# Kernel optimization log

Measured on AMD Instinct MI355X. Metric: run time of the kernel, lower is better.

Reference implementation:

```python
import jax, jax.numpy as jnp
import numpy as np

E = 1_000_000      # number of edges
N_NODE = 200_000   # nodes in this layer's frontier
IN_DIM = 64
ATTN_DIM = 64
OUT_DIM = 64
N_REL = 200
N_ENT = 50_000
B = 8              # batchsize


def setup_inputs() -> dict:
    key = jax.random.key(0)
    ks = jax.random.split(key, 16)
    # edges columns: [r_idx, _, rel, _, sub, obj]
    r_idx = jax.random.randint(ks[0], (E,), 0, B)
    rel = jax.random.randint(ks[1], (E,), 0, 2 * N_REL + 1)
    sub = jax.random.randint(ks[2], (E,), 0, N_NODE)
    obj = jax.random.randint(ks[3], (E,), 0, N_NODE)
    zeros = jnp.zeros((E,), dtype=jnp.int64 if jax.config.jax_enable_x64 else jnp.int32)
    edges = jnp.stack([r_idx, zeros, rel, zeros, sub, obj], axis=1)

    q_sub = jax.random.randint(ks[4], (B,), 0, N_ENT)
    q_rel = jax.random.randint(ks[5], (B,), 0, 2 * N_REL + 1)
    hidden = jax.random.normal(ks[6], (N_NODE, IN_DIM), dtype=jnp.float32)
    nodes = jnp.stack([jax.random.randint(ks[7], (N_NODE,), 0, B),
                       jax.random.randint(ks[8], (N_NODE,), 0, N_ENT)], axis=1)
    old_nodes_new_idx = jnp.sort(jax.random.randint(ks[9], (N_NODE // 2,), 0, N_NODE))

    s = 1.0 / np.sqrt(IN_DIM)
    rela_embed = jax.random.normal(ks[10], (2 * N_REL + 1, IN_DIM), dtype=jnp.float32)
    Ws = jax.random.uniform(ks[11], (ATTN_DIM, IN_DIM), minval=-s, maxval=s)  # Ws_attn.weight
    Wr = jax.random.uniform(ks[12], (ATTN_DIM, IN_DIM), minval=-s, maxval=s)  # Wr_attn.weight
    Wqr_W = jax.random.uniform(ks[13], (ATTN_DIM, IN_DIM), minval=-s, maxval=s)
    Wqr_b = jax.random.uniform(ks[14], (ATTN_DIM,), minval=-s, maxval=s)
    sa = 1.0 / np.sqrt(ATTN_DIM)
    kk = jax.random.split(ks[15], 3)
    wa_W = jax.random.uniform(kk[0], (1, ATTN_DIM), minval=-sa, maxval=sa)  # w_alpha.weight
    wa_b = jax.random.uniform(kk[1], (1,), minval=-sa, maxval=sa)
    Wh = jax.random.uniform(kk[2], (OUT_DIM, IN_DIM), minval=-s, maxval=s)  # W_h.weight

    return {"q_sub": q_sub, "q_rel": q_rel, "hidden": hidden, "edges": edges,
            "nodes": nodes, "old_nodes_new_idx": old_nodes_new_idx, "batchsize": B,
            "rela_embed": rela_embed, "Ws": Ws, "Wr": Wr, "Wqr_W": Wqr_W,
            "Wqr_b": Wqr_b, "wa_W": wa_W, "wa_b": wa_b, "Wh": Wh}


def reference(q_sub, q_rel, hidden, edges, nodes, old_nodes_new_idx, batchsize,
              rela_embed, Ws, Wr, Wqr_W, Wqr_b, wa_W, wa_b, Wh):
    sub = edges[:, 4]
    rel = edges[:, 2]
    obj = edges[:, 5]
    r_idx = edges[:, 0]
    n_node = nodes.shape[0]

    hs = hidden[sub]                      # [E, in_dim] gather
    hr = rela_embed[rel]                  # [E, in_dim]
    h_qr = rela_embed[q_rel][r_idx]       # [E, in_dim]

    # attention MLP: relu(Ws hs + Wr hr + Wqr h_qr + b) -> scalar -> sigmoid gate
    attn_input = (jnp.einsum('ei,ai->ea', hs, Ws)
                  + jnp.einsum('ei,ai->ea', hr, Wr)
                  + jnp.einsum('ei,ai->ea', h_qr, Wqr_W) + Wqr_b)  # [E, attn_dim]
    alpha = jax.nn.sigmoid(jax.nn.relu(attn_input) @ wa_W.T + wa_b)  # [E, 1]

    message = alpha * (hs + hr)                                       # [E, in_dim]
    message_agg = jax.ops.segment_sum(message, obj, num_segments=n_node)  # [n_node, in_dim]
    hidden_new = message_agg @ Wh.T  # act is identity (default)
    return hidden_new
```

## Files before the change

### kernel.cpp

```cpp
#include <hip/hip_runtime.h>
#include <hip/hip_bf16.h>


__global__ __launch_bounds__(256) void rowproj64(const float* src,
                                                 const float* __restrict__ W,
                                                 float* dst, int nrows) {
    __shared__ float Wt[64][65];
    __shared__ float4 Sl[64][16];
    int tid = threadIdx.x;
    for (int i = tid; i < 4096; i += 256) Wt[i & 63][i >> 6] = W[i];
    long r0 = (long)blockIdx.x * 64;
    const float4* src4 = (const float4*)(src + r0 * 64);
    float4* s4 = (float4*)Sl;
    for (int i = tid; i < 1024; i += 256) s4[i] = src4[i];
    __syncthreads();
    int c = tid & 63;
    int rbase = (tid >> 6) * 16;
    float w[64];
#pragma unroll
    for (int k = 0; k < 64; ++k) w[k] = Wt[k][c];
#pragma unroll
    for (int r = 0; r < 16; ++r) {
        float a0 = 0.f, a1 = 0.f, a2 = 0.f, a3 = 0.f;
#pragma unroll
        for (int k4 = 0; k4 < 16; ++k4) {
            float4 s = Sl[rbase + r][k4];
            a0 += s.x * w[4 * k4 + 0];
            a1 += s.y * w[4 * k4 + 1];
            a2 += s.z * w[4 * k4 + 2];
            a3 += s.w * w[4 * k4 + 3];
        }
        dst[(r0 + rbase + r) * 64 + c] = (a0 + a1) + (a2 + a3);
    }
}

__global__ void k_ct(const float* __restrict__ rela,
                     const int* __restrict__ q_rel,
                     const float* __restrict__ Wr,
                     const float* __restrict__ Wqr,
                     const float* __restrict__ bqr,
                     float* __restrict__ ct, int B) {
    int rel = blockIdx.x, a = threadIdx.x;
    __shared__ float hr[64];
    __shared__ float hq[8][64];
    hr[a] = rela[(size_t)rel * 64 + a];
    for (int b = 0; b < B; ++b) hq[b][a] = rela[(size_t)q_rel[b] * 64 + a];
    __syncthreads();
    float accr = 0.f;
#pragma unroll
    for (int k = 0; k < 64; ++k) accr += hr[k] * Wr[a * 64 + k];
    for (int b = 0; b < B; ++b) {
        float acc = bqr[a];
#pragma unroll
        for (int k = 0; k < 64; ++k) acc += hq[b][k] * Wqr[a * 64 + k];
        ct[((size_t)rel * 8 + b) * 64 + a] = accr + acc;
    }
}

__global__ void k_count(const int* __restrict__ edges, int E,
                        int* __restrict__ deg, int* __restrict__ rank) {
    int e = blockIdx.x * blockDim.x + threadIdx.x;
    if (e < E) rank[e] = atomicAdd(&deg[edges[(size_t)e * 6 + 5]], 1);
}

#define SCAN_BS 256
__global__ __launch_bounds__(SCAN_BS) void k_scan_block(
    const int* __restrict__ deg, int N,
    int* __restrict__ rowptr, int* __restrict__ bsum) {
    __shared__ int sh[SCAN_BS];
    int t = threadIdx.x, b = blockIdx.x;
    int base = b * 1024 + t * 4;
    int d0 = (base + 0 < N) ? deg[base + 0] : 0;
    int d1 = (base + 1 < N) ? deg[base + 1] : 0;
    int d2 = (base + 2 < N) ? deg[base + 2] : 0;
    int d3 = (base + 3 < N) ? deg[base + 3] : 0;
    int s = d0 + d1 + d2 + d3;
    sh[t] = s;
    __syncthreads();
    for (int o = 1; o < SCAN_BS; o <<= 1) {
        int v = (t >= o) ? sh[t - o] : 0;
        __syncthreads();
        sh[t] += v;
        __syncthreads();
    }
    int run = sh[t] - s;
    if (t == SCAN_BS - 1) bsum[b] = sh[t];
    if (base + 0 < N) rowptr[base + 0] = run;  run += d0;
    if (base + 1 < N) rowptr[base + 1] = run;  run += d1;
    if (base + 2 < N) rowptr[base + 2] = run;  run += d2;
    if (base + 3 < N) rowptr[base + 3] = run;
}

__global__ __launch_bounds__(SCAN_BS) void k_scan_partials(
    const int* __restrict__ bsum, int* __restrict__ boffs, int NB) {
    __shared__ int sh[SCAN_BS];
    int t = threadIdx.x;
    int v = (t < NB) ? bsum[t] : 0;
    sh[t] = v;
    __syncthreads();
    for (int o = 1; o < SCAN_BS; o <<= 1) {
        int u = (t >= o) ? sh[t - o] : 0;
        __syncthreads();
        sh[t] += u;
        __syncthreads();
    }
    if (t < NB) boffs[t] = sh[t] - v;
}

__global__ void k_add_offsets(int* __restrict__ rowptr,
                              const int* __restrict__ boffs, int N, int E) {
    int i = blockIdx.x * blockDim.x + threadIdx.x;
    if (i < N) rowptr[i] += boffs[i >> 10];
    if (i == 0) rowptr[N] = E;
}

__global__ void k_key(const int* __restrict__ edges, int E,
                      const int* __restrict__ rowptr,
                      const int* __restrict__ rank,
                      unsigned int* __restrict__ key) {
    int e = blockIdx.x * blockDim.x + threadIdx.x;
    if (e >= E) return;
    const int* ed = edges + (size_t)e * 6;
    int r_idx = ed[0], rel = ed[2], sub = ed[4], obj = ed[5];
    int pos = rowptr[obj] + rank[e];
    key[pos] = (unsigned int)sub | ((unsigned int)(rel * 8 + r_idx) << 18);
}

__global__ __launch_bounds__(256) void k_agg(
    const int* __restrict__ rowptr,
    const unsigned int* __restrict__ key,
    const float* __restrict__ hproj,
    const float* __restrict__ ct,
    const float* __restrict__ hidden,
    const float* __restrict__ rela,
    const float* __restrict__ wa,
    const float* __restrict__ wab_p,
    float* __restrict__ agg, int N) {
    int lane = threadIdx.x & 63;
    int half = lane >> 5;
    int li   = lane & 31;
    int w = (int)((blockIdx.x * blockDim.x + threadIdx.x) >> 6);
    if (w >= N) return;
    int n = __builtin_amdgcn_readfirstlane(w);
    int s = rowptr[n], e = rowptr[n + 1];
    const float2* hproj2  = (const float2*)hproj;
    const float2* ct2     = (const float2*)ct;
    const float2* hidden2 = (const float2*)hidden;
    const float2* rela2   = (const float2*)rela;
    float2 wav = ((const float2*)wa)[li];
    float wab = wab_p[0];
    float2 acc = {0.f, 0.f};

    if (s < e) {
        int j1c = min(s + 1, e - 1);
        unsigned int ka = key[s], kb = key[j1c];
        unsigned int kk = half ? kb : ka;
        float vld = (half == 0 || s + 1 < e) ? 1.f : 0.f;
        int sub = (int)(kk & 0x3FFFFu);
        int cr  = (int)(kk >> 18);
        float2 hp = hproj2[(size_t)sub * 32 + li];
        float2 cv = ct2[(size_t)cr * 32 + li];
        float2 hd = hidden2[(size_t)sub * 32 + li];
        float2 rl = rela2[(size_t)(cr >> 3) * 32 + li];

        for (int j = s + 2; j < e; j += 2) {
            int j1n = min(j + 1, e - 1);
            unsigned int ka1 = key[j], kb1 = key[j1n];
            unsigned int kk1 = half ? kb1 : ka1;
            float vld1 = (half == 0 || j + 1 < e) ? 1.f : 0.f;
            int sub1 = (int)(kk1 & 0x3FFFFu);
            int cr1  = (int)(kk1 >> 18);
            float2 hp1 = hproj2[(size_t)sub1 * 32 + li];
            float2 cv1 = ct2[(size_t)cr1 * 32 + li];
            float2 hd1 = hidden2[(size_t)sub1 * 32 + li];
            float2 rl1 = rela2[(size_t)(cr1 >> 3) * 32 + li];
            float t = fmaxf(hp.x + cv.x, 0.f) * wav.x
                    + fmaxf(hp.y + cv.y, 0.f) * wav.y;
#pragma unroll
            for (int o = 16; o; o >>= 1) t += __shfl_xor(t, o, 64);
            float am = vld / (1.f + __expf(-(t + wab)));
            acc.x += am * (hd.x + rl.x);
            acc.y += am * (hd.y + rl.y);
            hp = hp1; cv = cv1; hd = hd1; rl = rl1; vld = vld1;
        }
        float t = fmaxf(hp.x + cv.x, 0.f) * wav.x
                + fmaxf(hp.y + cv.y, 0.f) * wav.y;
#pragma unroll
        for (int o = 16; o; o >>= 1) t += __shfl_xor(t, o, 64);
        float am = vld / (1.f + __expf(-(t + wab)));
        acc.x += am * (hd.x + rl.x);
        acc.y += am * (hd.y + rl.y);
    }
    acc.x += __shfl_xor(acc.x, 32, 64);
    acc.y += __shfl_xor(acc.y, 32, 64);
    if (half == 0) ((float2*)agg)[(size_t)n * 32 + li] = acc;
}

extern "C" void kernel_launch(void* const* d_in, const int* in_sizes, int n_in,
                              void* d_out, int out_size, void* d_ws, size_t ws_size,
                              hipStream_t stream) {
    const int* q_rel    = (const int*)d_in[1];
    const float* hidden = (const float*)d_in[2];
    const int* edges    = (const int*)d_in[3];
    const float* rela   = (const float*)d_in[7];
    const float* Ws     = (const float*)d_in[8];
    const float* Wr     = (const float*)d_in[9];
    const float* WqrW   = (const float*)d_in[10];
    const float* Wqrb   = (const float*)d_in[11];
    const float* waW    = (const float*)d_in[12];
    const float* wab    = (const float*)d_in[13];
    const float* Wh     = (const float*)d_in[14];

    int E = in_sizes[3] / 6;
    int n_node = in_sizes[4] / 2;
    int n_rel_tot = in_sizes[7] / 64;
    int B = in_sizes[0];
    int NB = (n_node + 1023) / 1024;

    float* agg = (float*)d_out;
    char* w = (char*)d_ws;
    float* hproj = (float*)w;                  w += (size_t)n_node * 64 * 4;
    float* ct    = (float*)w;                  w += (size_t)n_rel_tot * 8 * 64 * 4;
    unsigned int* key = (unsigned int*)w;      w += (size_t)E * 4;
    int* rank   = (int*)w;                     w += (size_t)E * 4;
    int* deg    = (int*)w;                     w += (size_t)n_node * 4;
    int* rowptr = (int*)w;                     w += (size_t)(n_node + 1) * 4;
    int* bsum   = (int*)w;                     w += (size_t)NB * 4;
    int* boffs  = (int*)w;                     w += (size_t)NB * 4;

    rowproj64<<<n_node / 64, 256, 0, stream>>>(hidden, Ws, hproj, n_node);
    k_ct<<<n_rel_tot, 64, 0, stream>>>(rela, q_rel, Wr, WqrW, Wqrb, ct, B);

    hipMemsetAsync(deg, 0, (size_t)n_node * 4, stream);
    k_count<<<(E + 255) / 256, 256, 0, stream>>>(edges, E, deg, rank);
    k_scan_block<<<NB, SCAN_BS, 0, stream>>>(deg, n_node, rowptr, bsum);
    k_scan_partials<<<1, SCAN_BS, 0, stream>>>(bsum, boffs, NB);
    k_add_offsets<<<(n_node + 255) / 256, 256, 0, stream>>>(rowptr, boffs,
                                                            n_node, E);

    k_key<<<(E + 255) / 256, 256, 0, stream>>>(edges, E, rowptr, rank, key);
    k_agg<<<(n_node * 64 + 255) / 256, 256, 0, stream>>>(
        rowptr, key, hproj, ct, hidden, rela, waW, wab, agg, n_node);
    rowproj64<<<n_node / 64, 256, 0, stream>>>(agg, Wh, agg, n_node);
}
```

Before: 401.7 us.

## Fuse CSR build into one cooperative kernel and store attention projections as bf16

Replaces the memset, count, three scan kernels and key-scatter kernel with a single cooperative kernel that uses grid-wide syncs. This removes several launch gaps and intermediate passes. Separately, the hidden-projection and relation/query constant tables are stored in bf16, which halves the gathered bytes per edge for the attention logit in the aggregation kernel. The cost is lower precision in the gate logit, plus the rigid grid of 512 blocks that the cooperative launch requires.

```diff
diff --git a/kernel.cpp b/kernel.cpp
--- a/kernel.cpp
+++ b/kernel.cpp
@@ -1,6 +1,15 @@
 #include <hip/hip_runtime.h>
 #include <hip/hip_bf16.h>
-
+#include <hip/hip_cooperative_groups.h>
+
+namespace cg = cooperative_groups;
+
+
+__device__ __forceinline__ unsigned short f2bf(float f) {
+    unsigned int u = __float_as_uint(f);
+    u += 0x7FFF + ((u >> 16) & 1);
+    return (unsigned short)(u >> 16);
+}
 
 __global__ __launch_bounds__(256) void rowproj64(const float* src,
                                                  const float* __restrict__ W,
@@ -34,12 +43,45 @@
     }
 }
 
+__global__ __launch_bounds__(256) void rowproj_bf16(const float* __restrict__ src,
+                                                    const float* __restrict__ W,
+                                                    unsigned short* __restrict__ dst,
+                                                    int nrows) {
+    __shared__ float Wt[64][65];
+    __shared__ float4 Sl[64][16];
+    int tid = threadIdx.x;
+    for (int i = tid; i < 4096; i += 256) Wt[i & 63][i >> 6] = W[i];
+    long r0 = (long)blockIdx.x * 64;
+    const float4* src4 = (const float4*)(src + r0 * 64);
+    float4* s4 = (float4*)Sl;
+    for (int i = tid; i < 1024; i += 256) s4[i] = src4[i];
+    __syncthreads();
+    int c = tid & 63;
+    int rbase = (tid >> 6) * 16;
+    float w[64];
+#pragma unroll
+    for (int k = 0; k < 64; ++k) w[k] = Wt[k][c];
+#pragma unroll
+    for (int r = 0; r < 16; ++r) {
+        float a0 = 0.f, a1 = 0.f, a2 = 0.f, a3 = 0.f;
+#pragma unroll
+        for (int k4 = 0; k4 < 16; ++k4) {
+            float4 s = Sl[rbase + r][k4];
+            a0 += s.x * w[4 * k4 + 0];
+            a1 += s.y * w[4 * k4 + 1];
+            a2 += s.z * w[4 * k4 + 2];
+            a3 += s.w * w[4 * k4 + 3];
+        }
+        dst[(r0 + rbase + r) * 64 + c] = f2bf((a0 + a1) + (a2 + a3));
+    }
+}
+
 __global__ void k_ct(const float* __restrict__ rela,
                      const int* __restrict__ q_rel,
                      const float* __restrict__ Wr,
                      const float* __restrict__ Wqr,
                      const float* __restrict__ bqr,
-                     float* __restrict__ ct, int B) {
+                     unsigned short* __restrict__ ct, int B) {
     int rel = blockIdx.x, a = threadIdx.x;
     __shared__ float hr[64];
     __shared__ float hq[8][64];
@@ -53,84 +95,102 @@
         float acc = bqr[a];
 #pragma unroll
         for (int k = 0; k < 64; ++k) acc += hq[b][k] * Wqr[a * 64 + k];
-        ct[((size_t)rel * 8 + b) * 64 + a] = accr + acc;
-    }
-}
-
-__global__ void k_count(const int* __restrict__ edges, int E,
-                        int* __restrict__ deg, int* __restrict__ rank) {
-    int e = blockIdx.x * blockDim.x + threadIdx.x;
-    if (e < E) rank[e] = atomicAdd(&deg[edges[(size_t)e * 6 + 5]], 1);
-}
-
-#define SCAN_BS 256
-__global__ __launch_bounds__(SCAN_BS) void k_scan_block(
-    const int* __restrict__ deg, int N,
-    int* __restrict__ rowptr, int* __restrict__ bsum) {
-    __shared__ int sh[SCAN_BS];
-    int t = threadIdx.x, b = blockIdx.x;
-    int base = b * 1024 + t * 4;
-    int d0 = (base + 0 < N) ? deg[base + 0] : 0;
-    int d1 = (base + 1 < N) ? deg[base + 1] : 0;
-    int d2 = (base + 2 < N) ? deg[base + 2] : 0;
-    int d3 = (base + 3 < N) ? deg[base + 3] : 0;
-    int s = d0 + d1 + d2 + d3;
-    sh[t] = s;
-    __syncthreads();
-    for (int o = 1; o < SCAN_BS; o <<= 1) {
-        int v = (t >= o) ? sh[t - o] : 0;
+        ct[((size_t)rel * 8 + b) * 64 + a] = f2bf(accr + acc);
+    }
+}
+
+__global__ __launch_bounds__(256, 2) void k_csr(
+    const int* __restrict__ edges, int E, int N,
+    int* __restrict__ deg, int* __restrict__ rank,
+    int* __restrict__ partial, int* __restrict__ poffs,
+    int* __restrict__ rowptr, unsigned int* __restrict__ key) {
+    cg::grid_group grid = cg::this_grid();
+    __shared__ int smem[1024];
+    int t = threadIdx.x;
+    int b = blockIdx.x;
+    int gid = b * 256 + t;
+    const int GSTRIDE = 512 * 256;
+    int nchunk = (N + 511) >> 9;
+
+    for (int i = gid; i < N; i += GSTRIDE) deg[i] = 0;
+    grid.sync();
+
+    for (int e = gid; e < E; e += GSTRIDE)
+        rank[e] = atomicAdd(&deg[edges[(size_t)e * 6 + 5]], 1);
+    grid.sync();
+
+    if (b < nchunk) {
+        int c0 = b << 9;
+        int v = 0;
+        int i0 = c0 + t;       if (i0 < N) v = deg[i0];
+        int i1 = c0 + t + 256; if (i1 < N) v += deg[i1];
+        smem[t] = v;
         __syncthreads();
-        sh[t] += v;
+        for (int o = 128; o; o >>= 1) {
+            if (t < o) smem[t] += smem[t + o];
+            __syncthreads();
+        }
+        if (t == 0) partial[b] = smem[0];
+    } else if (t == 0) {
+        partial[b] = 0;
+    }
+    grid.sync();
+
+    if (b == 0) {
+        int* A = smem;
+        int* Bb = smem + 512;
+        int o0 = partial[t], o1 = partial[t + 256];
+        A[t] = o0; A[t + 256] = o1;
         __syncthreads();
-    }
-    int run = sh[t] - s;
-    if (t == SCAN_BS - 1) bsum[b] = sh[t];
-    if (base + 0 < N) rowptr[base + 0] = run;  run += d0;
-    if (base + 1 < N) rowptr[base + 1] = run;  run += d1;
-    if (base + 2 < N) rowptr[base + 2] = run;  run += d2;
-    if (base + 3 < N) rowptr[base + 3] = run;
-}
-
-__global__ __launch_bounds__(SCAN_BS) void k_scan_partials(
-    const int* __restrict__ bsum, int* __restrict__ boffs, int NB) {
-    __shared__ int sh[SCAN_BS];
-    int t = threadIdx.x;
-    int v = (t < NB) ? bsum[t] : 0;
-    sh[t] = v;
-    __syncthreads();
-    for (int o = 1; o < SCAN_BS; o <<= 1) {
-        int u = (t >= o) ? sh[t - o] : 0;
+        for (int o = 1; o < 512; o <<= 1) {
+            Bb[t] = A[t] + (t >= o ? A[t - o] : 0);
+            int i2 = t + 256;
+            Bb[i2] = A[i2] + (i2 >= o ? A[i2 - o] : 0);
+            __syncthreads();
+            int* tmp = A; A = Bb; Bb = tmp;
+        }
+        poffs[t] = A[t] - o0;
+        poffs[t + 256] = A[t + 256] - o1;
+    }
+    grid.sync();
+
+    if (b < nchunk) {
+        int c0 = b << 9;
+        int i0 = c0 + 2 * t, i1 = i0 + 1;
+        int d0 = (i0 < N) ? deg[i0] : 0;
+        int d1 = (i1 < N) ? deg[i1] : 0;
+        int ps = d0 + d1;
+        int* A = smem;
+        int* Bb = smem + 256;
+        A[t] = ps;
         __syncthreads();
-        sh[t] += u;
-        __syncthreads();
-    }
-    if (t < NB) boffs[t] = sh[t] - v;
-}
-
-__global__ void k_add_offsets(int* __restrict__ rowptr,
-                              const int* __restrict__ boffs, int N, int E) {
-    int i = blockIdx.x * blockDim.x + threadIdx.x;
-    if (i < N) rowptr[i] += boffs[i >> 10];
-    if (i == 0) rowptr[N] = E;
-}
-
-__global__ void k_key(const int* __restrict__ edges, int E,
-                      const int* __restrict__ rowptr,
-                      const int* __restrict__ rank,
-                      unsigned int* __restrict__ key) {
-    int e = blockIdx.x * blockDim.x + threadIdx.x;
-    if (e >= E) return;
-    const int* ed = edges + (size_t)e * 6;
-    int r_idx = ed[0], rel = ed[2], sub = ed[4], obj = ed[5];
-    int pos = rowptr[obj] + rank[e];
-    key[pos] = (unsigned int)sub | ((unsigned int)(rel * 8 + r_idx) << 18);
+        for (int o = 1; o < 256; o <<= 1) {
+            Bb[t] = A[t] + (t >= o ? A[t - o] : 0);
+            __syncthreads();
+            int* tmp = A; A = Bb; Bb = tmp;
+        }
+        int base = poffs[b] + A[t] - ps;
+        if (i0 < N) rowptr[i0] = base;
+        if (i1 < N) rowptr[i1] = base + d0;
+    }
+    if (gid == 0) rowptr[N] = E;
+    grid.sync();
+
+    for (int e = gid; e < E; e += GSTRIDE) {
+        const int* ed = edges + (size_t)e * 6;
+        int2 p0 = *(const int2*)(ed);
+        int2 p1 = *(const int2*)(ed + 2);
+        int2 p2 = *(const int2*)(ed + 4);
+        int pos = rowptr[p2.y] + rank[e];
+        key[pos] = (unsigned int)p2.x | ((unsigned int)(p1.x * 8 + p0.x) << 18);
+    }
 }
 
 __global__ __launch_bounds__(256) void k_agg(
     const int* __restrict__ rowptr,
     const unsigned int* __restrict__ key,
-    const float* __restrict__ hproj,
-    const float* __restrict__ ct,
+    const unsigned short* __restrict__ hproj16,
+    const unsigned short* __restrict__ ct16,
     const float* __restrict__ hidden,
     const float* __restrict__ rela,
     const float* __restrict__ wa,
@@ -143,8 +203,8 @@
     if (w >= N) return;
     int n = __builtin_amdgcn_readfirstlane(w);
     int s = rowptr[n], e = rowptr[n + 1];
-    const float2* hproj2  = (const float2*)hproj;
-    const float2* ct2     = (const float2*)ct;
+    const unsigned int* hp2 = (const unsigned int*)hproj16;
+    const unsigned int* ct2 = (const unsigned int*)ct16;
     const float2* hidden2 = (const float2*)hidden;
     const float2* rela2   = (const float2*)rela;
     float2 wav = ((const float2*)wa)[li];
@@ -158,8 +218,8 @@
         float vld = (half == 0 || s + 1 < e) ? 1.f : 0.f;
         int sub = (int)(kk & 0x3FFFFu);
         int cr  = (int)(kk >> 18);
-        float2 hp = hproj2[(size_t)sub * 32 + li];
-        float2 cv = ct2[(size_t)cr * 32 + li];
+        unsigned int hpu = hp2[(size_t)sub * 32 + li];
+        unsigned int cvu = ct2[(size_t)cr * 32 + li];
         float2 hd = hidden2[(size_t)sub * 32 + li];
         float2 rl = rela2[(size_t)(cr >> 3) * 32 + li];
 
@@ -170,24 +230,33 @@
             float vld1 = (half == 0 || j + 1 < e) ? 1.f : 0.f;
             int sub1 = (int)(kk1 & 0x3FFFFu);
             int cr1  = (int)(kk1 >> 18);
-            float2 hp1 = hproj2[(size_t)sub1 * 32 + li];
-            float2 cv1 = ct2[(size_t)cr1 * 32 + li];
+            unsigned int hpu1 = hp2[(size_t)sub1 * 32 + li];
+            unsigned int cvu1 = ct2[(size_t)cr1 * 32 + li];
             float2 hd1 = hidden2[(size_t)sub1 * 32 + li];
             float2 rl1 = rela2[(size_t)(cr1 >> 3) * 32 + li];
-            float t = fmaxf(hp.x + cv.x, 0.f) * wav.x
-                    + fmaxf(hp.y + cv.y, 0.f) * wav.y;
-#pragma unroll
-            for (int o = 16; o; o >>= 1) t += __shfl_xor(t, o, 64);
-            float am = vld / (1.f + __expf(-(t + wab)));
+
+            float hpx = __uint_as_float(hpu << 16);
+            float hpy = __uint_as_float(hpu & 0xFFFF0000u);
+            float cvx = __uint_as_float(cvu << 16);
+            float cvy = __uint_as_float(cvu & 0xFFFF0000u);
+            float tt = fmaxf(hpx + cvx, 0.f) * wav.x
+                     + fmaxf(hpy + cvy, 0.f) * wav.y;
+#pragma unroll
+            for (int o = 16; o; o >>= 1) tt += __shfl_xor(tt, o, 64);
+            float am = vld / (1.f + __expf(-(tt + wab)));
             acc.x += am * (hd.x + rl.x);
             acc.y += am * (hd.y + rl.y);
-            hp = hp1; cv = cv1; hd = hd1; rl = rl1; vld = vld1;
-        }
-        float t = fmaxf(hp.x + cv.x, 0.f) * wav.x
-                + fmaxf(hp.y + cv.y, 0.f) * wav.y;
-#pragma unroll
-        for (int o = 16; o; o >>= 1) t += __shfl_xor(t, o, 64);
-        float am = vld / (1.f + __expf(-(t + wab)));
+            hpu = hpu1; cvu = cvu1; hd = hd1; rl = rl1; vld = vld1;
+        }
+        float hpx = __uint_as_float(hpu << 16);
+        float hpy = __uint_as_float(hpu & 0xFFFF0000u);
+        float cvx = __uint_as_float(cvu << 16);
+        float cvy = __uint_as_float(cvu & 0xFFFF0000u);
+        float tt = fmaxf(hpx + cvx, 0.f) * wav.x
+                 + fmaxf(hpy + cvy, 0.f) * wav.y;
+#pragma unroll
+        for (int o = 16; o; o >>= 1) tt += __shfl_xor(tt, o, 64);
+        float am = vld / (1.f + __expf(-(tt + wab)));
         acc.x += am * (hd.x + rl.x);
         acc.y += am * (hd.y + rl.y);
     }
@@ -215,31 +284,28 @@
     int n_node = in_sizes[4] / 2;
     int n_rel_tot = in_sizes[7] / 64;
     int B = in_sizes[0];
-    int NB = (n_node + 1023) / 1024;
 
     float* agg = (float*)d_out;
     char* w = (char*)d_ws;
-    float* hproj = (float*)w;                  w += (size_t)n_node * 64 * 4;
-    float* ct    = (float*)w;                  w += (size_t)n_rel_tot * 8 * 64 * 4;
-    unsigned int* key = (unsigned int*)w;      w += (size_t)E * 4;
-    int* rank   = (int*)w;                     w += (size_t)E * 4;
-    int* deg    = (int*)w;                     w += (size_t)n_node * 4;
-    int* rowptr = (int*)w;                     w += (size_t)(n_node + 1) * 4;
-    int* bsum   = (int*)w;                     w += (size_t)NB * 4;
-    int* boffs  = (int*)w;                     w += (size_t)NB * 4;
-
-    rowproj64<<<n_node / 64, 256, 0, stream>>>(hidden, Ws, hproj, n_node);
-    k_ct<<<n_rel_tot, 64, 0, stream>>>(rela, q_rel, Wr, WqrW, Wqrb, ct, B);
-
-    hipMemsetAsync(deg, 0, (size_t)n_node * 4, stream);
-    k_count<<<(E + 255) / 256, 256, 0, stream>>>(edges, E, deg, rank);
-    k_scan_block<<<NB, SCAN_BS, 0, stream>>>(deg, n_node, rowptr, bsum);
-    k_scan_partials<<<1, SCAN_BS, 0, stream>>>(bsum, boffs, NB);
-    k_add_offsets<<<(n_node + 255) / 256, 256, 0, stream>>>(rowptr, boffs,
-                                                            n_node, E);
-
-    k_key<<<(E + 255) / 256, 256, 0, stream>>>(edges, E, rowptr, rank, key);
+    unsigned short* hproj16 = (unsigned short*)w;  w += (size_t)n_node * 64 * 2;
+    unsigned short* ct16    = (unsigned short*)w;  w += (size_t)n_rel_tot * 8 * 64 * 2;
+    unsigned int* key = (unsigned int*)w;          w += (size_t)E * 4;
+    int* rank    = (int*)w;                        w += (size_t)E * 4;
+    int* deg     = (int*)w;                        w += (size_t)n_node * 4;
+    int* rowptr  = (int*)w;                        w += (size_t)(n_node + 1) * 4;
+    int* partial = (int*)w;                        w += 512 * 4;
+    int* poffs   = (int*)w;                        w += 512 * 4;
+
+    rowproj_bf16<<<n_node / 64, 256, 0, stream>>>(hidden, Ws, hproj16, n_node);
+    k_ct<<<n_rel_tot, 64, 0, stream>>>(rela, q_rel, Wr, WqrW, Wqrb, ct16, B);
+
+    void* args[] = {(void*)&edges, (void*)&E, (void*)&n_node,
+                    (void*)&deg, (void*)&rank, (void*)&partial,
+                    (void*)&poffs, (void*)&rowptr, (void*)&key};
+    hipLaunchCooperativeKernel((const void*)k_csr, dim3(512), dim3(256),
+                               args, 0, stream);
+
     k_agg<<<(n_node * 64 + 255) / 256, 256, 0, stream>>>(
-        rowptr, key, hproj, ct, hidden, rela, waW, wab, agg, n_node);
+        rowptr, key, hproj16, ct16, hidden, rela, waW, wab, agg, n_node);
     rowproj64<<<n_node / 64, 256, 0, stream>>>(agg, Wh, agg, n_node);
 }
```

Measured after the change: 675.1 us. +68.1%, slower.

## Store attention projections in bf16 and process four edges per wave in aggregation

Applied to the files above, without the earlier changes.

The node projection (hidden·Wsᵀ) and the relation/query constant table are now stored as bf16, which halves the bytes gathered per edge for the attention logit. The aggregation kernel splits each wave into four 16-lane groups so four edges are handled per iteration with float4/uint2 loads, followed by a wider final reduction. The deg zeroing is folded into the projection kernel, replacing a separate memset. The cost is reduced precision in the attention pre-activation and more shuffle work per edge.

```diff
diff --git a/kernel.cpp b/kernel.cpp
--- a/kernel.cpp
+++ b/kernel.cpp
@@ -1,6 +1,12 @@
 #include <hip/hip_runtime.h>
 #include <hip/hip_bf16.h>
 
+
+__device__ __forceinline__ unsigned short f2bf(float f) {
+    unsigned int u = __float_as_uint(f);
+    u += 0x7FFF + ((u >> 16) & 1);
+    return (unsigned short)(u >> 16);
+}
 
 __global__ __launch_bounds__(256) void rowproj64(const float* src,
                                                  const float* __restrict__ W,
@@ -34,12 +40,47 @@
     }
 }
 
+__global__ __launch_bounds__(256) void rowproj_bf16(const float* __restrict__ src,
+                                                    const float* __restrict__ W,
+                                                    unsigned short* __restrict__ dst,
+                                                    int* __restrict__ deg,
+                                                    int nrows) {
+    __shared__ float Wt[64][65];
+    __shared__ float4 Sl[64][16];
+    int tid = threadIdx.x;
+    long r0 = (long)blockIdx.x * 64;
+    if (tid < 64 && r0 + tid < nrows) deg[r0 + tid] = 0;
+    for (int i = tid; i < 4096; i += 256) Wt[i & 63][i >> 6] = W[i];
+    const float4* src4 = (const float4*)(src + r0 * 64);
+    float4* s4 = (float4*)Sl;
+    for (int i = tid; i < 1024; i += 256) s4[i] = src4[i];
+    __syncthreads();
+    int c = tid & 63;
+    int rbase = (tid >> 6) * 16;
+    float w[64];
+#pragma unroll
+    for (int k = 0; k < 64; ++k) w[k] = Wt[k][c];
+#pragma unroll
+    for (int r = 0; r < 16; ++r) {
+        float a0 = 0.f, a1 = 0.f, a2 = 0.f, a3 = 0.f;
+#pragma unroll
+        for (int k4 = 0; k4 < 16; ++k4) {
+            float4 s = Sl[rbase + r][k4];
+            a0 += s.x * w[4 * k4 + 0];
+            a1 += s.y * w[4 * k4 + 1];
+            a2 += s.z * w[4 * k4 + 2];
+            a3 += s.w * w[4 * k4 + 3];
+        }
+        dst[(r0 + rbase + r) * 64 + c] = f2bf((a0 + a1) + (a2 + a3));
+    }
+}
+
 __global__ void k_ct(const float* __restrict__ rela,
                      const int* __restrict__ q_rel,
                      const float* __restrict__ Wr,
                      const float* __restrict__ Wqr,
                      const float* __restrict__ bqr,
-                     float* __restrict__ ct, int B) {
+                     unsigned short* __restrict__ ct, int B) {
     int rel = blockIdx.x, a = threadIdx.x;
     __shared__ float hr[64];
     __shared__ float hq[8][64];
@@ -53,7 +94,7 @@
         float acc = bqr[a];
 #pragma unroll
         for (int k = 0; k < 64; ++k) acc += hq[b][k] * Wqr[a * 64 + k];
-        ct[((size_t)rel * 8 + b) * 64 + a] = accr + acc;
+        ct[((size_t)rel * 8 + b) * 64 + a] = f2bf(accr + acc);
     }
 }
 
@@ -129,71 +170,87 @@
 __global__ __launch_bounds__(256) void k_agg(
     const int* __restrict__ rowptr,
     const unsigned int* __restrict__ key,
-    const float* __restrict__ hproj,
-    const float* __restrict__ ct,
+    const unsigned short* __restrict__ hproj16,
+    const unsigned short* __restrict__ ct16,
     const float* __restrict__ hidden,
     const float* __restrict__ rela,
     const float* __restrict__ wa,
     const float* __restrict__ wab_p,
     float* __restrict__ agg, int N) {
     int lane = threadIdx.x & 63;
-    int half = lane >> 5;
-    int li   = lane & 31;
+    int g  = lane >> 4;
+    int li = lane & 15;
     int w = (int)((blockIdx.x * blockDim.x + threadIdx.x) >> 6);
     if (w >= N) return;
     int n = __builtin_amdgcn_readfirstlane(w);
     int s = rowptr[n], e = rowptr[n + 1];
-    const float2* hproj2  = (const float2*)hproj;
-    const float2* ct2     = (const float2*)ct;
-    const float2* hidden2 = (const float2*)hidden;
-    const float2* rela2   = (const float2*)rela;
-    float2 wav = ((const float2*)wa)[li];
+    const uint2* hp2 = (const uint2*)hproj16;
+    const uint2* ct2 = (const uint2*)ct16;
+    const float4* hidden4 = (const float4*)hidden;
+    const float4* rela4   = (const float4*)rela;
+    float4 wav = ((const float4*)wa)[li];
     float wab = wab_p[0];
-    float2 acc = {0.f, 0.f};
+    float4 acc = {0.f, 0.f, 0.f, 0.f};
+
+#define LOADK(J, KK, VLD, SUB, CR, HPU, CVU, HD, RL)                          \
+    {                                                                         \
+        int j1 = min((J) + 1, e - 1), j2 = min((J) + 2, e - 1),               \
+            j3 = min((J) + 3, e - 1);                                         \
+        unsigned int k0 = key[(J)], k1 = key[j1], k2 = key[j2], k3 = key[j3]; \
+        unsigned int ka = (g & 1) ? k1 : k0, kb = (g & 1) ? k3 : k2;          \
+        KK = (g & 2) ? kb : ka;                                               \
+        VLD = ((J) + g < e) ? 1.f : 0.f;                                      \
+        SUB = (int)(KK & 0x3FFFFu);                                           \
+        CR = (int)(KK >> 18);                                                 \
+        HPU = hp2[(size_t)SUB * 16 + li];                                     \
+        CVU = ct2[(size_t)CR * 16 + li];                                      \
+        HD = hidden4[(size_t)SUB * 16 + li];                                  \
+        RL = rela4[(size_t)(CR >> 3) * 16 + li];                              \
+    }
+
+#define CONSUME(VLD, HPU, CVU, HD, RL)                                        \
+    {                                                                         \
+        float h0 = __uint_as_float(HPU.x << 16);                              \
+        float h1 = __uint_as_float(HPU.x & 0xFFFF0000u);                      \
+        float h2 = __uint_as_float(HPU.y << 16);                              \
+        float h3 = __uint_as_float(HPU.y & 0xFFFF0000u);                      \
+        float c0 = __uint_as_float(CVU.x << 16);                              \
+        float c1 = __uint_as_float(CVU.x & 0xFFFF0000u);                      \
+        float c2 = __uint_as_float(CVU.y << 16);                              \
+        float c3 = __uint_as_float(CVU.y & 0xFFFF0000u);                      \
+        float tt = fmaxf(h0 + c0, 0.f) * wav.x + fmaxf(h1 + c1, 0.f) * wav.y  \
+                 + fmaxf(h2 + c2, 0.f) * wav.z + fmaxf(h3 + c3, 0.f) * wav.w; \
+        tt += __shfl_xor(tt, 8, 64);                                          \
+        tt += __shfl_xor(tt, 4, 64);                                          \
+        tt += __shfl_xor(tt, 2, 64);                                          \
+        tt += __shfl_xor(tt, 1, 64);                                          \
+        float am = VLD / (1.f + __expf(-(tt + wab)));                         \
+        acc.x += am * (HD.x + RL.x);                                          \
+        acc.y += am * (HD.y + RL.y);                                          \
+        acc.z += am * (HD.z + RL.z);                                          \
+        acc.w += am * (HD.w + RL.w);                                          \
+    }
 
     if (s < e) {
-        int j1c = min(s + 1, e - 1);
-        unsigned int ka = key[s], kb = key[j1c];
-        unsigned int kk = half ? kb : ka;
-        float vld = (half == 0 || s + 1 < e) ? 1.f : 0.f;
-        int sub = (int)(kk & 0x3FFFFu);
-        int cr  = (int)(kk >> 18);
-        float2 hp = hproj2[(size_t)sub * 32 + li];
-        float2 cv = ct2[(size_t)cr * 32 + li];
-        float2 hd = hidden2[(size_t)sub * 32 + li];
-        float2 rl = rela2[(size_t)(cr >> 3) * 32 + li];
-
-        for (int j = s + 2; j < e; j += 2) {
-            int j1n = min(j + 1, e - 1);
-            unsigned int ka1 = key[j], kb1 = key[j1n];
-            unsigned int kk1 = half ? kb1 : ka1;
-            float vld1 = (half == 0 || j + 1 < e) ? 1.f : 0.f;
-            int sub1 = (int)(kk1 & 0x3FFFFu);
-            int cr1  = (int)(kk1 >> 18);
-            float2 hp1 = hproj2[(size_t)sub1 * 32 + li];
-            float2 cv1 = ct2[(size_t)cr1 * 32 + li];
-            float2 hd1 = hidden2[(size_t)sub1 * 32 + li];
-            float2 rl1 = rela2[(size_t)(cr1 >> 3) * 32 + li];
-            float t = fmaxf(hp.x + cv.x, 0.f) * wav.x
-                    + fmaxf(hp.y + cv.y, 0.f) * wav.y;
-#pragma unroll
-            for (int o = 16; o; o >>= 1) t += __shfl_xor(t, o, 64);
-            float am = vld / (1.f + __expf(-(t + wab)));
-            acc.x += am * (hd.x + rl.x);
-            acc.y += am * (hd.y + rl.y);
-            hp = hp1; cv = cv1; hd = hd1; rl = rl1; vld = vld1;
+        unsigned int kk; float vld; int sub, cr;
+        uint2 hpu, cvu; float4 hd, rl;
+        LOADK(s, kk, vld, sub, cr, hpu, cvu, hd, rl);
+        for (int j = s + 4; j < e; j += 4) {
+            unsigned int kk1; float vld1; int sub1, cr1;
+            uint2 hpu1, cvu1; float4 hd1, rl1;
+            LOADK(j, kk1, vld1, sub1, cr1, hpu1, cvu1, hd1, rl1);
+            CONSUME(vld, hpu, cvu, hd, rl);
+            hpu = hpu1; cvu = cvu1; hd = hd1; rl = rl1; vld = vld1;
         }
-        float t = fmaxf(hp.x + cv.x, 0.f) * wav.x
-                + fmaxf(hp.y + cv.y, 0.f) * wav.y;
-#pragma unroll
-        for (int o = 16; o; o >>= 1) t += __shfl_xor(t, o, 64);
-        float am = vld / (1.f + __expf(-(t + wab)));
-        acc.x += am * (hd.x + rl.x);
-        acc.y += am * (hd.y + rl.y);
-    }
-    acc.x += __shfl_xor(acc.x, 32, 64);
-    acc.y += __shfl_xor(acc.y, 32, 64);
-    if (half == 0) ((float2*)agg)[(size_t)n * 32 + li] = acc;
+        CONSUME(vld, hpu, cvu, hd, rl);
+    }
+    acc.x += __shfl_xor(acc.x, 16, 64);  acc.x += __shfl_xor(acc.x, 32, 64);
+    acc.y += __shfl_xor(acc.y, 16, 64);  acc.y += __shfl_xor(acc.y, 32, 64);
+    acc.z += __shfl_xor(acc.z, 16, 64);  acc.z += __shfl_xor(acc.z, 32, 64);
+    acc.w += __shfl_xor(acc.w, 16, 64);  acc.w += __shfl_xor(acc.w, 32, 64);
+    if (g == 0) ((float4*)agg)[(size_t)n * 16 + li] = acc;
+#undef LOADK
+#undef CONSUME
 }
 
 extern "C" void kernel_launch(void* const* d_in, const int* in_sizes, int n_in,
@@ -219,27 +276,26 @@
 
     float* agg = (float*)d_out;
     char* w = (char*)d_ws;
-    float* hproj = (float*)w;                  w += (size_t)n_node * 64 * 4;
-    float* ct    = (float*)w;                  w += (size_t)n_rel_tot * 8 * 64 * 4;
-    unsigned int* key = (unsigned int*)w;      w += (size_t)E * 4;
-    int* rank   = (int*)w;                     w += (size_t)E * 4;
-    int* deg    = (int*)w;                     w += (size_t)n_node * 4;
-    int* rowptr = (int*)w;                     w += (size_t)(n_node + 1) * 4;
-    int* bsum   = (int*)w;                     w += (size_t)NB * 4;
-    int* boffs  = (int*)w;                     w += (size_t)NB * 4;
-
-    rowproj64<<<n_node / 64, 256, 0, stream>>>(hidden, Ws, hproj, n_node);
-    k_ct<<<n_rel_tot, 64, 0, stream>>>(rela, q_rel, Wr, WqrW, Wqrb, ct, B);
-
-    hipMemsetAsync(deg, 0, (size_t)n_node * 4, stream);
+    unsigned short* hproj16 = (unsigned short*)w;  w += (size_t)n_node * 64 * 2;
+    unsigned short* ct16    = (unsigned short*)w;  w += (size_t)n_rel_tot * 8 * 64 * 2;
+    unsigned int* key = (unsigned int*)w;          w += (size_t)E * 4;
+    int* rank   = (int*)w;                         w += (size_t)E * 4;
+    int* deg    = (int*)w;                         w += (size_t)n_node * 4;
+    int* rowptr = (int*)w;                         w += (size_t)(n_node + 1) * 4;
+    int* bsum   = (int*)w;                         w += (size_t)NB * 4;
+    int* boffs  = (int*)w;                         w += (size_t)NB * 4;
+
+    rowproj_bf16<<<n_node / 64, 256, 0, stream>>>(hidden, Ws, hproj16, deg, n_node);
+    k_ct<<<n_rel_tot, 64, 0, stream>>>(rela, q_rel, Wr, WqrW, Wqrb, ct16, B);
+
     k_count<<<(E + 255) / 256, 256, 0, stream>>>(edges, E, deg, rank);
     k_scan_block<<<NB, SCAN_BS, 0, stream>>>(deg, n_node, rowptr, bsum);
     k_scan_partials<<<1, SCAN_BS, 0, stream>>>(bsum, boffs, NB);
     k_add_offsets<<<(n_node + 255) / 256, 256, 0, stream>>>(rowptr, boffs,
                                                             n_node, E);
-
     k_key<<<(E + 255) / 256, 256, 0, stream>>>(edges, E, rowptr, rank, key);
+
     k_agg<<<(n_node * 64 + 255) / 256, 256, 0, stream>>>(
-        rowptr, key, hproj, ct, hidden, rela, waW, wab, agg, n_node);
+        rowptr, key, hproj16, ct16, hidden, rela, waW, wab, agg, n_node);
     rowproj64<<<n_node / 64, 256, 0, stream>>>(agg, Wh, agg, n_node);
 }
```

Measured after the change: 393.1 us. 2.1% less time.
